# Optimization experiments

Measured on AMD Instinct MI355X. Metric: run time of the kernel, lower is better.

Reference implementation:

```python
import jax, jax.numpy as jnp
import numpy as np

N = 50000   # nodes
E = 800000  # edges (avg degree 16)
D = 128     # in_feats == out_feats


def setup_inputs() -> dict:
    key = jax.random.key(0)
    k1, k2, k3, k4 = jax.random.split(key, 4)
    h = jax.random.normal(k1, (N, D), dtype=jnp.float32)
    src = jax.random.randint(k2, (E,), 0, N, dtype=jnp.int32)
    dst = jax.random.randint(k3, (E,), 0, N, dtype=jnp.int32)
    snorm_n = jnp.ones((N, 1), dtype=jnp.float32)  # sqrt(1/N) replicated; identity-scaled here
    # NodeApply linear: Linear(2*D, D) with bias
    W = jax.random.normal(k4, (D, 2 * D), dtype=jnp.float32) / np.sqrt(2 * D).astype(np.float32)
    b = jnp.zeros((D,), dtype=jnp.float32)
    return {"h": h, "snorm_n": snorm_n, "W": W, "b": b, "src": src, "dst": dst}


def reference(h, snorm_n, W, b, src, dst):
    # dropout p=0.0 -> identity
    h_in = h
    # gather neighbor messages and segment-mean aggregate (MeanAggregator)
    ones = jnp.ones((src.shape[0],), dtype=h.dtype)
    deg = jax.ops.segment_sum(ones, dst, num_segments=N)            # [N]
    msg_sum = jax.ops.segment_sum(h[src], dst, num_segments=N)     # [N, D]
    c = msg_sum / jnp.maximum(deg, 1.0)[:, None]                   # zero-degree nodes -> c = 0
    # NodeApply: concat -> linear -> L2 normalize -> relu
    bundle = jnp.concatenate([h, c], axis=1) @ W.T + b             # [N, D]
    nrm = jnp.sqrt(jnp.sum(bundle * bundle, axis=1, keepdims=True))
    bundle = bundle / jnp.maximum(nrm, 1e-12)                      # F.normalize(p=2, dim=1)
    out = jax.nn.relu(bundle)
    # graph norm
    out = out * snorm_n
    # residual (in_feats == out_feats)
    return h_in + out
```

## Files before the change

kernel.cpp:

```cpp
#include <hip/hip_runtime.h>
#include <hip/hip_bf16.h>

#define TPB 256
#define CHUNK_LOG 13
#define CHUNK (1 << CHUNK_LOG)
#define HSTRIDE 12544

typedef __attribute__((ext_vector_type(8))) short bf16x8;
typedef __attribute__((ext_vector_type(4))) float f32x4;

__device__ inline unsigned short f2bf(float f) {
    unsigned u = __float_as_uint(f);
    unsigned r = u + 0x7fffu + ((u >> 16) & 1u);
    return (unsigned short)(r >> 16);
}
__device__ inline float bf2f(unsigned short s) {
    return __uint_as_float(((unsigned)s) << 16);
}

__global__ void k_conv(const float* __restrict__ h, const float* __restrict__ W,
                       unsigned short* __restrict__ h_hi,
                       unsigned short* __restrict__ Wb, int N) {
    int t = blockIdx.x * TPB + threadIdx.x;
    int nh4 = N * 32;
    if (t < nh4) {
        float4 v = ((const float4*)h)[t];
        ushort4 hi;
        hi.x = f2bf(v.x); hi.y = f2bf(v.y);
        hi.z = f2bf(v.z); hi.w = f2bf(v.w);
        ((ushort4*)h_hi)[t] = hi;
    } else if (t - nh4 < 8192) {
        int w4 = t - nh4;
        float4 v = ((const float4*)W)[w4];
        ushort4 hi;
        hi.x = f2bf(v.x); hi.y = f2bf(v.y);
        hi.z = f2bf(v.z); hi.w = f2bf(v.w);
        ((ushort4*)Wb)[w4] = hi;
    }
}

__global__ void k_hist(const int* __restrict__ dst,
                       unsigned* __restrict__ hist32, unsigned char* __restrict__ lrank,
                       int E) {
    __shared__ unsigned lhist[HSTRIDE];
    int b = blockIdx.x;
    for (int i = threadIdx.x; i < HSTRIDE; i += TPB) lhist[i] = 0;
    __syncthreads();
    int e0 = b << CHUNK_LOG;
    int e1 = min(e0 + CHUNK, E);
    for (int e = e0 + (int)threadIdx.x; e < e1; e += TPB) {
        int d = dst[e];
        unsigned sh = (d & 3) * 8;
        unsigned old = atomicAdd(&lhist[d >> 2], 1u << sh);
        lrank[e] = (unsigned char)((old >> sh) & 0xffu);
    }
    __syncthreads();
    for (int i = threadIdx.x; i < HSTRIDE; i += TPB)
        hist32[(size_t)b * HSTRIDE + i] = lhist[i];
}

__global__ void k_colscan(const unsigned* __restrict__ hist32,
                          unsigned short* __restrict__ cbase, int* __restrict__ deg,
                          int* __restrict__ bsum, int N, int NBH) {
    extern __shared__ unsigned tile[];
    __shared__ int sdata[4];
    int tileBase = blockIdx.x * 64;
    int total = NBH * 64;
    for (int i = threadIdx.x; i < total; i += TPB) {
        int b = i >> 6, c = i & 63;
        tile[i] = hist32[(size_t)b * HSTRIDE + tileBase + c];
    }
    __syncthreads();
    int t = threadIdx.x;
    int n = blockIdx.x * TPB + t;
    unsigned sh = (t & 3) * 8;
    int wcol = t >> 2;
    int run = 0;
    for (int b = 0; b < NBH; ++b) {
        int c = (int)((tile[b * 64 + wcol] >> sh) & 0xffu);
        if (n < N) cbase[(size_t)b * N + n] = (unsigned short)run;
        run += c;
    }
    if (n < N) deg[n] = run; else run = 0;
    int s = run;
    for (int o = 32; o; o >>= 1) s += __shfl_xor(s, o);
    int lane = t & 63, w = t >> 6;
    if (lane == 0) sdata[w] = s;
    __syncthreads();
    if (t == 0) bsum[blockIdx.x] = sdata[0] + sdata[1] + sdata[2] + sdata[3];
}

__global__ void k_offs2(const int* __restrict__ deg, const int* __restrict__ bsum,
                        int* __restrict__ offs, int N, int E) {
    __shared__ int sb[TPB];
    __shared__ int wsum[4];
    int NB = gridDim.x;
    int t = threadIdx.x;
    int lane = t & 63, w = t >> 6;
    int v = (t < NB) ? bsum[t] : 0;
    int x = v;
    for (int o = 1; o < 64; o <<= 1) { int y = __shfl_up(x, o); if (lane >= o) x += y; }
    if (lane == 63) wsum[w] = x;
    __syncthreads();
    int add = 0;
    for (int k = 0; k < w; ++k) add += wsum[k];
    sb[t] = add + x - v;
    __syncthreads();
    int base = sb[blockIdx.x];
    int i = blockIdx.x * TPB + t;
    int dv = (i < N) ? deg[i] : 0;
    int y2 = dv;
    for (int o = 1; o < 64; o <<= 1) { int z = __shfl_up(y2, o); if (lane >= o) y2 += z; }
    __syncthreads();
    if (lane == 63) wsum[w] = y2;
    __syncthreads();
    int add2 = 0;
    for (int k = 0; k < w; ++k) add2 += wsum[k];
    int ex = base + add2 + y2 - dv;
    if (i < N) offs[i] = ex;
    if (i == N - 1) offs[N] = E;
}

__global__ void k_scatter(const int* __restrict__ src, const int* __restrict__ dst,
                          const unsigned char* __restrict__ lrank,
                          const unsigned short* __restrict__ cbase,
                          const int* __restrict__ offs,
                          unsigned short* __restrict__ esrc, int N, int E, int nchunk) {
    int slice = blockIdx.x & 7;
    int chunk = blockIdx.x >> 3;
    int lo = (int)((long long)N * slice >> 3);
    int hi = (int)((long long)N * (slice + 1) >> 3);
    for (int e = chunk * TPB + threadIdx.x; e < E; e += nchunk * TPB) {
        int d = dst[e];
        if (d >= lo && d < hi) {
            int b = e >> CHUNK_LOG;
            int pos = offs[d] + (int)cbase[(size_t)b * N + d] + (int)lrank[e];
            esrc[pos] = (unsigned short)src[e];
        }
    }
}

__global__ void k_agg(const unsigned short* __restrict__ h_hi, const int* __restrict__ offs,
                      const unsigned short* __restrict__ esrc,
                      unsigned* __restrict__ c, int N) {
    int wid = (blockIdx.x * TPB + threadIdx.x) >> 6;
    int lane = threadIdx.x & 63;
    if (wid >= N) return;
    int beg = offs[wid], end = offs[wid + 1];
    const unsigned* h2 = (const unsigned*)h_hi;
    float ax0 = 0.f, ay0 = 0.f, ax1 = 0.f, ay1 = 0.f;
    int e = beg;
    for (; e + 3 < end; e += 4) {
        int s0 = esrc[e], s1 = esrc[e + 1], s2 = esrc[e + 2], s3 = esrc[e + 3];
        unsigned u0 = h2[(size_t)s0 * 64 + lane];
        unsigned u1 = h2[(size_t)s1 * 64 + lane];
        unsigned u2 = h2[(size_t)s2 * 64 + lane];
        unsigned u3 = h2[(size_t)s3 * 64 + lane];
        ax0 += __uint_as_float(u0 << 16) + __uint_as_float(u1 << 16);
        ay0 += __uint_as_float(u0 & 0xffff0000u) + __uint_as_float(u1 & 0xffff0000u);
        ax1 += __uint_as_float(u2 << 16) + __uint_as_float(u3 << 16);
        ay1 += __uint_as_float(u2 & 0xffff0000u) + __uint_as_float(u3 & 0xffff0000u);
    }
    for (; e < end; ++e) {
        unsigned u0 = h2[(size_t)esrc[e] * 64 + lane];
        ax0 += __uint_as_float(u0 << 16);
        ay0 += __uint_as_float(u0 & 0xffff0000u);
    }
    float ax = ax0 + ax1, ay = ay0 + ay1;
    float inv = 1.0f / fmaxf((float)(end - beg), 1.0f);
    unsigned pk = ((unsigned)f2bf(ay * inv) << 16) | (unsigned)f2bf(ax * inv);
    c[(size_t)wid * 64 + lane] = pk;
}

__launch_bounds__(TPB)
__global__ void k_apply(const unsigned short* __restrict__ h_hi,
                        const unsigned short* __restrict__ c,
                        const unsigned short* __restrict__ Wb,
                        const float* __restrict__ bia,
                        const float* __restrict__ snorm,
                        float* __restrict__ out, int N) {
    int lane = threadIdx.x & 63;
    int l15 = lane & 15, l4 = lane >> 4;
    int wave = threadIdx.x >> 6;
    int r0 = blockIdx.x * 128 + wave * 32;

    f32x4 acc[2][8] = {};

    #pragma unroll
    for (int kc = 0; kc < 8; ++kc) {
        bf16x8 Bf[8];
        #pragma unroll
        for (int n = 0; n < 8; ++n) {
            Bf[n] = *(const bf16x8*)((const char*)Wb +
                     ((size_t)(n * 16 + l15) * 512 + (size_t)kc * 64 + (size_t)l4 * 16));
        }
        #pragma unroll
        for (int rf = 0; rf < 2; ++rf) {
            int row = r0 + rf * 16 + l15;
            if (row > N - 1) row = N - 1;
            bf16x8 av;
            if (kc < 4) {
                av = *(const bf16x8*)((const char*)h_hi +
                      ((size_t)row * 256 + (size_t)kc * 64 + (size_t)l4 * 16));
            } else {
                av = *(const bf16x8*)((const char*)c +
                      ((size_t)row * 256 + (size_t)(kc - 4) * 64 + (size_t)l4 * 16));
            }
            #pragma unroll
            for (int n = 0; n < 8; ++n)
                acc[rf][n] = __builtin_amdgcn_mfma_f32_16x16x32_bf16(av, Bf[n], acc[rf][n], 0, 0, 0);
        }
    }

    float bn[8];
    #pragma unroll
    for (int n = 0; n < 8; ++n) bn[n] = bia[n * 16 + l15];

    #pragma unroll
    for (int rf = 0; rf < 2; ++rf) {
        float sq[4] = {0.f, 0.f, 0.f, 0.f};
        #pragma unroll
        for (int n = 0; n < 8; ++n) {
            #pragma unroll
            for (int g = 0; g < 4; ++g) {
                acc[rf][n][g] += bn[n];
                sq[g] += acc[rf][n][g] * acc[rf][n][g];
            }
        }
        #pragma unroll
        for (int g = 0; g < 4; ++g) {
            sq[g] += __shfl_xor(sq[g], 1);
            sq[g] += __shfl_xor(sq[g], 2);
            sq[g] += __shfl_xor(sq[g], 4);
            sq[g] += __shfl_xor(sq[g], 8);
        }
        #pragma unroll
        for (int g = 0; g < 4; ++g) {
            int row = r0 + rf * 16 + l4 * 4 + g;
            if (row < N) {
                float invn = 1.0f / fmaxf(sqrtf(sq[g]), 1e-12f);
                float sn = snorm[row];
                #pragma unroll
                for (int n = 0; n < 8; ++n) {
                    int col = n * 16 + l15;
                    float res = bf2f(h_hi[(size_t)row * 128 + col]);
                    out[(size_t)row * 128 + col] =
                        fmaxf(acc[rf][n][g] * invn, 0.f) * sn + res;
                }
            }
        }
    }
}

extern "C" void kernel_launch(void* const* d_in, const int* in_sizes, int n_in,
                              void* d_out, int out_size, void* d_ws, size_t ws_size,
                              hipStream_t stream) {
    const float* h     = (const float*)d_in[0];
    const float* snorm = (const float*)d_in[1];
    const float* W     = (const float*)d_in[2];
    const float* b     = (const float*)d_in[3];
    const int*   src   = (const int*)d_in[4];
    const int*   dst   = (const int*)d_in[5];
    int N = in_sizes[1];
    int E = in_sizes[4];
    float* out = (float*)d_out;

    char* ws = (char*)d_ws;
    size_t off = 0;
    auto alloc = [&](size_t bytes) {
        void* ptr = ws + off;
        off = (off + bytes + 255) & ~(size_t)255;
        return ptr;
    };
    int NB  = (N + TPB - 1) / TPB;
    int NBH = (E + CHUNK - 1) >> CHUNK_LOG;
    int* deg    = (int*)alloc((size_t)N * 4);
    int* offs   = (int*)alloc((size_t)(N + 1) * 4);
    int* bsum   = (int*)alloc((size_t)NB * 4);
    unsigned* hist32       = (unsigned*)alloc((size_t)NBH * HSTRIDE * 4);
    unsigned short* cbase  = (unsigned short*)alloc((size_t)NBH * N * 2);
    unsigned char*  lrank  = (unsigned char*)alloc((size_t)E);
    unsigned short* esrc   = (unsigned short*)alloc((size_t)E * 2);
    unsigned short* h_hi   = (unsigned short*)alloc((size_t)N * 128 * 2);
    unsigned short* Wb     = (unsigned short*)alloc((size_t)128 * 256 * 2);
    unsigned* c = hist32;

    int conv_blocks = (N * 32 + 8192 + TPB - 1) / TPB;
    k_conv<<<conv_blocks, TPB, 0, stream>>>(h, W, h_hi, Wb, N);

    k_hist<<<NBH, TPB, 0, stream>>>(dst, hist32, lrank, E);

    size_t tile_bytes = (size_t)NBH * 64 * 4;
    k_colscan<<<NB, TPB, tile_bytes, stream>>>(hist32, cbase, deg, bsum, N, NBH);
    k_offs2<<<NB, TPB, 0, stream>>>(deg, bsum, offs, N, E);

    int nchunk = 512;
    k_scatter<<<8 * nchunk, TPB, 0, stream>>>(src, dst, lrank, cbase, offs, esrc, N, E, nchunk);

    k_agg<<<((size_t)N * 64 + TPB - 1) / TPB, TPB, 0, stream>>>(h_hi, offs, esrc, c, N);

    int nblk = (N + 127) / 128;
    k_apply<<<nblk, TPB, 0, stream>>>(h_hi, (const unsigned short*)c, Wb, b, snorm, out, N);
}
```

Measured before the change: 114.1 us.

## Fuse CSR build kernels into one cooperative kernel with grid syncs

Replaces five separate launches (bf16 conversion, histogram, column scan, offset scan, scatter) with a single cooperative kernel of 512 blocks that uses grid-wide barriers between phases. The bf16 conversion is moved to the end, after the scatter. The aim is to remove per-launch overhead and inter-kernel gaps in the graph-build preamble. In exchange the scatter now runs on far fewer blocks (512 instead of 4096), and grid.sync has its own cost. The 49KB of shared memory per block may also limit how many blocks fit for a cooperative launch.

```diff
diff --git a/kernel.cpp b/kernel.cpp
--- a/kernel.cpp
+++ b/kernel.cpp
@@ -1,10 +1,14 @@
 #include <hip/hip_runtime.h>
 #include <hip/hip_bf16.h>
+#include <hip/hip_cooperative_groups.h>
+
+namespace cg = cooperative_groups;
 
 #define TPB 256
 #define CHUNK_LOG 13
 #define CHUNK (1 << CHUNK_LOG)
 #define HSTRIDE 12544
+#define BUILD_GRID 512
 
 typedef __attribute__((ext_vector_type(8))) short bf16x8;
 typedef __attribute__((ext_vector_type(4))) float f32x4;
@@ -18,124 +22,128 @@
     return __uint_as_float(((unsigned)s) << 16);
 }
 
-__global__ void k_conv(const float* __restrict__ h, const float* __restrict__ W,
-                       unsigned short* __restrict__ h_hi,
-                       unsigned short* __restrict__ Wb, int N) {
-    int t = blockIdx.x * TPB + threadIdx.x;
-    int nh4 = N * 32;
-    if (t < nh4) {
-        float4 v = ((const float4*)h)[t];
-        ushort4 hi;
-        hi.x = f2bf(v.x); hi.y = f2bf(v.y);
-        hi.z = f2bf(v.z); hi.w = f2bf(v.w);
-        ((ushort4*)h_hi)[t] = hi;
-    } else if (t - nh4 < 8192) {
-        int w4 = t - nh4;
-        float4 v = ((const float4*)W)[w4];
-        ushort4 hi;
-        hi.x = f2bf(v.x); hi.y = f2bf(v.y);
-        hi.z = f2bf(v.z); hi.w = f2bf(v.w);
-        ((ushort4*)Wb)[w4] = hi;
-    }
-}
-
-__global__ void k_hist(const int* __restrict__ dst,
-                       unsigned* __restrict__ hist32, unsigned char* __restrict__ lrank,
-                       int E) {
-    __shared__ unsigned lhist[HSTRIDE];
-    int b = blockIdx.x;
-    for (int i = threadIdx.x; i < HSTRIDE; i += TPB) lhist[i] = 0;
-    __syncthreads();
-    int e0 = b << CHUNK_LOG;
-    int e1 = min(e0 + CHUNK, E);
-    for (int e = e0 + (int)threadIdx.x; e < e1; e += TPB) {
-        int d = dst[e];
-        unsigned sh = (d & 3) * 8;
-        unsigned old = atomicAdd(&lhist[d >> 2], 1u << sh);
-        lrank[e] = (unsigned char)((old >> sh) & 0xffu);
-    }
-    __syncthreads();
-    for (int i = threadIdx.x; i < HSTRIDE; i += TPB)
-        hist32[(size_t)b * HSTRIDE + i] = lhist[i];
-}
-
-__global__ void k_colscan(const unsigned* __restrict__ hist32,
-                          unsigned short* __restrict__ cbase, int* __restrict__ deg,
-                          int* __restrict__ bsum, int N, int NBH) {
-    extern __shared__ unsigned tile[];
-    __shared__ int sdata[4];
-    int tileBase = blockIdx.x * 64;
-    int total = NBH * 64;
-    for (int i = threadIdx.x; i < total; i += TPB) {
-        int b = i >> 6, c = i & 63;
-        tile[i] = hist32[(size_t)b * HSTRIDE + tileBase + c];
-    }
-    __syncthreads();
-    int t = threadIdx.x;
-    int n = blockIdx.x * TPB + t;
-    unsigned sh = (t & 3) * 8;
-    int wcol = t >> 2;
-    int run = 0;
-    for (int b = 0; b < NBH; ++b) {
-        int c = (int)((tile[b * 64 + wcol] >> sh) & 0xffu);
-        if (n < N) cbase[(size_t)b * N + n] = (unsigned short)run;
-        run += c;
-    }
-    if (n < N) deg[n] = run; else run = 0;
-    int s = run;
-    for (int o = 32; o; o >>= 1) s += __shfl_xor(s, o);
-    int lane = t & 63, w = t >> 6;
-    if (lane == 0) sdata[w] = s;
-    __syncthreads();
-    if (t == 0) bsum[blockIdx.x] = sdata[0] + sdata[1] + sdata[2] + sdata[3];
-}
-
-__global__ void k_offs2(const int* __restrict__ deg, const int* __restrict__ bsum,
-                        int* __restrict__ offs, int N, int E) {
-    __shared__ int sb[TPB];
-    __shared__ int wsum[4];
-    int NB = gridDim.x;
-    int t = threadIdx.x;
-    int lane = t & 63, w = t >> 6;
-    int v = (t < NB) ? bsum[t] : 0;
-    int x = v;
-    for (int o = 1; o < 64; o <<= 1) { int y = __shfl_up(x, o); if (lane >= o) x += y; }
-    if (lane == 63) wsum[w] = x;
-    __syncthreads();
-    int add = 0;
-    for (int k = 0; k < w; ++k) add += wsum[k];
-    sb[t] = add + x - v;
-    __syncthreads();
-    int base = sb[blockIdx.x];
-    int i = blockIdx.x * TPB + t;
-    int dv = (i < N) ? deg[i] : 0;
-    int y2 = dv;
-    for (int o = 1; o < 64; o <<= 1) { int z = __shfl_up(y2, o); if (lane >= o) y2 += z; }
-    __syncthreads();
-    if (lane == 63) wsum[w] = y2;
-    __syncthreads();
-    int add2 = 0;
-    for (int k = 0; k < w; ++k) add2 += wsum[k];
-    int ex = base + add2 + y2 - dv;
-    if (i < N) offs[i] = ex;
-    if (i == N - 1) offs[N] = E;
-}
-
-__global__ void k_scatter(const int* __restrict__ src, const int* __restrict__ dst,
-                          const unsigned char* __restrict__ lrank,
-                          const unsigned short* __restrict__ cbase,
-                          const int* __restrict__ offs,
-                          unsigned short* __restrict__ esrc, int N, int E, int nchunk) {
-    int slice = blockIdx.x & 7;
-    int chunk = blockIdx.x >> 3;
-    int lo = (int)((long long)N * slice >> 3);
-    int hi = (int)((long long)N * (slice + 1) >> 3);
-    for (int e = chunk * TPB + threadIdx.x; e < E; e += nchunk * TPB) {
-        int d = dst[e];
-        if (d >= lo && d < hi) {
-            int b = e >> CHUNK_LOG;
-            int pos = offs[d] + (int)cbase[(size_t)b * N + d] + (int)lrank[e];
-            esrc[pos] = (unsigned short)src[e];
+__launch_bounds__(TPB)
+__global__ void k_build(const float* __restrict__ h, const float* __restrict__ W,
+                        const int* __restrict__ src, const int* __restrict__ dst,
+                        unsigned short* __restrict__ h_hi, unsigned short* __restrict__ Wb,
+                        unsigned* __restrict__ hist32, unsigned char* __restrict__ lrank,
+                        unsigned short* __restrict__ cbase, int* __restrict__ deg,
+                        int* __restrict__ bsum, int* __restrict__ offs,
+                        unsigned short* __restrict__ esrc,
+                        int N, int E, int NBH, int NB) {
+    __shared__ unsigned lds[HSTRIDE];
+    cg::grid_group grid = cg::this_grid();
+    int tid = threadIdx.x;
+    int bid = blockIdx.x;
+    int lane = tid & 63, w = tid >> 6;
+
+    if (bid < NBH) {
+        for (int i = tid; i < HSTRIDE; i += TPB) lds[i] = 0;
+        __syncthreads();
+        int e0 = bid << CHUNK_LOG;
+        int e1 = min(e0 + CHUNK, E);
+        for (int e = e0 + tid; e < e1; e += TPB) {
+            int d = dst[e];
+            unsigned sh = (d & 3) * 8;
+            unsigned old = atomicAdd(&lds[d >> 2], 1u << sh);
+            lrank[e] = (unsigned char)((old >> sh) & 0xffu);
+        }
+        __syncthreads();
+        for (int i = tid; i < HSTRIDE; i += TPB)
+            hist32[(size_t)bid * HSTRIDE + i] = lds[i];
+    }
+    grid.sync();
+
+    if (bid < NB) {
+        unsigned* tile = lds;
+        int* sdata = (int*)&lds[12512];
+        int tileBase = bid * 64;
+        int total = NBH * 64;
+        for (int i = tid; i < total; i += TPB) {
+            int b = i >> 6, c = i & 63;
+            tile[i] = hist32[(size_t)b * HSTRIDE + tileBase + c];
+        }
+        __syncthreads();
+        int n = bid * TPB + tid;
+        unsigned sh = (tid & 3) * 8;
+        int wcol = tid >> 2;
+        int run = 0;
+        for (int b = 0; b < NBH; ++b) {
+            int c = (int)((tile[b * 64 + wcol] >> sh) & 0xffu);
+            if (n < N) cbase[(size_t)b * N + n] = (unsigned short)run;
+            run += c;
+        }
+        if (n < N) deg[n] = run; else run = 0;
+        int s = run;
+        for (int o = 32; o; o >>= 1) s += __shfl_xor(s, o);
+        if (lane == 0) sdata[w] = s;
+        __syncthreads();
+        if (tid == 0) bsum[bid] = sdata[0] + sdata[1] + sdata[2] + sdata[3];
+    }
+    grid.sync();
+
+    if (bid < NB) {
+        int* sb = (int*)lds;
+        int* wsum = (int*)&lds[12512];
+        int v = (tid < NB) ? bsum[tid] : 0;
+        int x = v;
+        for (int o = 1; o < 64; o <<= 1) { int y = __shfl_up(x, o); if (lane >= o) x += y; }
+        if (lane == 63) wsum[w] = x;
+        __syncthreads();
+        int add = 0;
+        for (int k = 0; k < w; ++k) add += wsum[k];
+        sb[tid] = add + x - v;
+        __syncthreads();
+        int base = sb[bid];
+        int i = bid * TPB + tid;
+        int dv = (i < N) ? deg[i] : 0;
+        int y2 = dv;
+        for (int o = 1; o < 64; o <<= 1) { int z = __shfl_up(y2, o); if (lane >= o) y2 += z; }
+        __syncthreads();
+        if (lane == 63) wsum[w] = y2;
+        __syncthreads();
+        int add2 = 0;
+        for (int k = 0; k < w; ++k) add2 += wsum[k];
+        int ex = base + add2 + y2 - dv;
+        if (i < N) offs[i] = ex;
+        if (i == N - 1) offs[N] = E;
+    }
+    grid.sync();
+
+    {
+        int slice = bid & 7;
+        int chunk = bid >> 3;
+        int nchunk = gridDim.x >> 3;
+        int lo = (int)((long long)N * slice >> 3);
+        int hi = (int)((long long)N * (slice + 1) >> 3);
+        for (int e = chunk * TPB + tid; e < E; e += nchunk * TPB) {
+            int d = dst[e];
+            if (d >= lo && d < hi) {
+                int b = e >> CHUNK_LOG;
+                int pos = offs[d] + (int)cbase[(size_t)b * N + d] + (int)lrank[e];
+                esrc[pos] = (unsigned short)src[e];
+            }
+        }
+    }
+
+    {
+        int nh4 = N * 32;
+        int total = nh4 + 8192;
+        for (int t = bid * TPB + tid; t < total; t += gridDim.x * TPB) {
+            if (t < nh4) {
+                float4 v = ((const float4*)h)[t];
+                ushort4 hi;
+                hi.x = f2bf(v.x); hi.y = f2bf(v.y);
+                hi.z = f2bf(v.z); hi.w = f2bf(v.w);
+                ((ushort4*)h_hi)[t] = hi;
+            } else {
+                int w4 = t - nh4;
+                float4 v = ((const float4*)W)[w4];
+                ushort4 hi;
+                hi.x = f2bf(v.x); hi.y = f2bf(v.y);
+                hi.z = f2bf(v.z); hi.w = f2bf(v.w);
+                ((ushort4*)Wb)[w4] = hi;
+            }
         }
     }
 }
@@ -285,17 +293,14 @@
     unsigned short* Wb     = (unsigned short*)alloc((size_t)128 * 256 * 2);
     unsigned* c = hist32;
 
-    int conv_blocks = (N * 32 + 8192 + TPB - 1) / TPB;
-    k_conv<<<conv_blocks, TPB, 0, stream>>>(h, W, h_hi, Wb, N);
-
-    k_hist<<<NBH, TPB, 0, stream>>>(dst, hist32, lrank, E);
-
-    size_t tile_bytes = (size_t)NBH * 64 * 4;
-    k_colscan<<<NB, TPB, tile_bytes, stream>>>(hist32, cbase, deg, bsum, N, NBH);
-    k_offs2<<<NB, TPB, 0, stream>>>(deg, bsum, offs, N, E);
-
-    int nchunk = 512;
-    k_scatter<<<8 * nchunk, TPB, 0, stream>>>(src, dst, lrank, cbase, offs, esrc, N, E, nchunk);
+    void* args[] = {
+        (void*)&h, (void*)&W, (void*)&src, (void*)&dst,
+        (void*)&h_hi, (void*)&Wb, (void*)&hist32, (void*)&lrank,
+        (void*)&cbase, (void*)&deg, (void*)&bsum, (void*)&offs,
+        (void*)&esrc, (void*)&N, (void*)&E, (void*)&NBH, (void*)&NB
+    };
+    hipLaunchCooperativeKernel((const void*)k_build, dim3(BUILD_GRID), dim3(TPB),
+                               args, 0, stream);
 
     k_agg<<<((size_t)N * 64 + TPB - 1) / TPB, TPB, 0, stream>>>(h_hi, offs, esrc, c, N);
 
```

New measurement: 288.1 us. 2.52x slower.
